# Optimization experiments

Hardware: AMD Instinct MI355X
Metric: run time of the kernel (lower is better)

Reference implementation:

```python
import jax, jax.numpy as jnp
import numpy as np

PAD = 26
H = 1900
B = 256
T_EPI = 25
T_ANT = 64
T_TOT = 153
EMB = 10
IC = 2 * H  # classifier in_channels = 3800


def setup_inputs() -> dict:
    key = jax.random.key(0)
    ks = jax.random.split(key, 16)
    def rn(i, s, sc):
        return jax.random.normal(ks[i], s, jnp.float32) * sc
    inp = {
        "epitope_x": jax.random.randint(ks[0], (B, T_EPI), 0, 26),
        "left_antigen_x": jax.random.randint(ks[1], (B, T_ANT), 0, 26),
        "right_antigen_x": jax.random.randint(ks[2], (B, T_ANT), 0, 26),
        "total_antigen_x": jax.random.randint(ks[3], (B, T_TOT), 0, 26),
        "embed": rn(4, (27, EMB), 0.1),
        "wx": rn(5, (EMB, 4 * H), 0.1),
        "wh": rn(6, (H, 4 * H), 0.02),
        "wmx": rn(7, (EMB, H), 0.1),
        "wmh": rn(8, (H, H), 0.02),
        "b": rn(9, (4 * H,), 0.1),
        "gx": jnp.ones((4 * H,), jnp.float32),
        "gh": jnp.ones((4 * H,), jnp.float32),
        "gmx": jnp.ones((H,), jnp.float32),
        "gmh": jnp.ones((H,), jnp.float32),
        "bn1_gamma": jnp.ones((IC,), jnp.float32),
        "bn1_beta": jnp.zeros((IC,), jnp.float32),
        "bn1_mean": jnp.zeros((IC,), jnp.float32),
        "bn1_var": jnp.ones((IC,), jnp.float32),
        "W1": rn(10, (IC, IC // 10), 0.02),
        "b1": jnp.zeros((IC // 10,), jnp.float32),
        "bn2_gamma": jnp.ones((IC // 10,), jnp.float32),
        "bn2_beta": jnp.zeros((IC // 10,), jnp.float32),
        "bn2_mean": jnp.zeros((IC // 10,), jnp.float32),
        "bn2_var": jnp.ones((IC // 10,), jnp.float32),
        "W2": rn(11, (IC // 10, 1), 0.05),
        "b2": jnp.zeros((1,), jnp.float32),
    }
    return inp


def _wn(w, g):
    # tf.nn.l2_normalize(w, dim=0) * g  (eps 1e-12)
    return w * (g * jax.lax.rsqrt(jnp.maximum(jnp.sum(w * w, axis=0, keepdims=True), 1e-12)))


def _mlstm(xs, wx, wh, wmx, wmh, b):
    # xs: [T, B, E] -> hidden states [B, T, H]
    nB = xs.shape[1]
    def step(carry, x):
        c, h = carry
        m = (x @ wmx) * (h @ wmh)
        z = x @ wx + m @ wh + b
        i, f, o, u = jnp.split(z, 4, axis=1)
        c = jax.nn.sigmoid(f) * c + jax.nn.sigmoid(i) * jnp.tanh(u)
        h = jax.nn.sigmoid(o) * jnp.tanh(c)
        return (c, h), h
    init = (jnp.zeros((nB, H), xs.dtype), jnp.zeros((nB, H), xs.dtype))
    _, hs = jax.lax.scan(step, init, xs)
    return jnp.swapaxes(hs, 0, 1)


def _forward(epitope_x, left_antigen_x, right_antigen_x, total_antigen_x, embed,
             wx, wh, wmx, wmh, b, gx, gh, gmx, gmh,
             bn1_gamma, bn1_beta, bn1_mean, bn1_var, W1, b1,
             bn2_gamma, bn2_beta, bn2_mean, bn2_var, W2, b2):
    wxn = _wn(wx, gx); whn = _wn(wh, gh); wmxn = _wn(wmx, gmx); wmhn = _wn(wmh, gmh)
    epi_len = jnp.sum((epitope_x != PAD).astype(jnp.int32), axis=1)
    left_len = jnp.maximum(jnp.sum((left_antigen_x != PAD).astype(jnp.int32), axis=1), 1)
    right_len = jnp.maximum(jnp.sum((right_antigen_x != PAD).astype(jnp.int32), axis=1), 1)
    tot_len = epi_len + left_len + right_len
    epi_emb = embed[epitope_x]          # [B, 25, 10]
    tot_emb = embed[total_antigen_x]    # [B, 153, 10]
    epi_hs = _mlstm(jnp.swapaxes(epi_emb, 0, 1), wxn, whn, wmxn, wmhn, b)   # [B, 25, H]
    tot_hs = _mlstm(jnp.swapaxes(tot_emb, 0, 1), wxn, whn, wmxn, wmhn, b)   # [B, 153, H]
    ei = jnp.clip(epi_len - 1, 0, epi_hs.shape[1] - 1)
    ti = jnp.clip(tot_len - 1, 0, tot_hs.shape[1] - 1)
    epi_h = jnp.take_along_axis(epi_hs, ei[:, None, None], axis=1)[:, 0]
    tot_h = jnp.take_along_axis(tot_hs, ti[:, None, None], axis=1)[:, 0]
    x = jnp.concatenate([tot_h, epi_h], axis=-1)  # [B, 3800]
    lrelu = lambda v: jnp.where(v >= 0, v, 0.3 * v)
    bn = lambda v, g, bt, m, vv: (v - m) * jax.lax.rsqrt(vv + 1e-3) * g + bt
    x = bn(lrelu(x), bn1_gamma, bn1_beta, bn1_mean, bn1_var)
    x = x @ W1 + b1
    x = bn(lrelu(x), bn2_gamma, bn2_beta, bn2_mean, bn2_var)
    x = x @ W2 + b2
    return x.reshape(-1)


def reference(epitope_x, left_antigen_x, right_antigen_x, total_antigen_x, embed,
              wx, wh, wmx, wmh, b, gx, gh, gmx, gmh,
              bn1_gamma, bn1_beta, bn1_mean, bn1_var, W1, b1,
              bn2_gamma, bn2_beta, bn2_mean, bn2_var, W2, b2):
    return _forward(epitope_x, left_antigen_x, right_antigen_x, total_antigen_x, embed,
                    wx, wh, wmx, wmh, b, gx, gh, gmx, gmh,
                    bn1_gamma, bn1_beta, bn1_mean, bn1_var, W1, b1,
                    bn2_gamma, bn2_beta, bn2_mean, bn2_var, W2, b2)
```

## Files before the change

kernel.cpp:

```cpp
#include <hip/hip_runtime.h>


typedef _Float16 f16;
typedef _Float16 half8 __attribute__((ext_vector_type(8)));
typedef float f32x4 __attribute__((ext_vector_type(4)));

#define H_    1900
#define HP    1920
#define NKA   60
#define NKB   61
#define NKF   120
#define NR    512
#define TT    153
#define TE    25
#define EMB_  10
#define FCN   384

__device__ __forceinline__ float sigm(float x) {
  float p = __expf(-fabsf(x));
  float r = 1.f / (1.f + p);
  return x >= 0.f ? r : 1.f - r;
}
__device__ __forceinline__ float tanh_(float x) {
  float p = __expf(-2.f * fabsf(x));
  float r = (1.f - p) / (1.f + p);
  return x >= 0.f ? r : -r;
}

__device__ __forceinline__ void gll16(const f16* g, f16* l) {
  __builtin_amdgcn_global_load_lds(
      (const __attribute__((address_space(1))) unsigned int*)g,
      (__attribute__((address_space(3))) unsigned int*)l, 16, 0, 0);
}


__global__ void k_norms(const float* __restrict__ wh, const float* __restrict__ wx,
                        const float* __restrict__ wmh, const float* __restrict__ wmx,
                        const float* __restrict__ gh, const float* __restrict__ gx,
                        const float* __restrict__ gmh, const float* __restrict__ gmx,
                        float* __restrict__ inv_wh, float* __restrict__ inv_wx,
                        float* __restrict__ inv_wmh, float* __restrict__ inv_wmx) {
  int tid = blockIdx.x * 256 + threadIdx.x;
  if (tid < 7600) {
    float s = 0.f;
    for (int k = 0; k < H_; k++) { float v = wh[(size_t)k * 7600 + tid]; s += v * v; }
    inv_wh[tid] = gh[tid] * rsqrtf(fmaxf(s, 1e-12f));
  } else if (tid < 15200) {
    int n = tid - 7600; float s = 0.f;
    for (int e = 0; e < EMB_; e++) { float v = wx[(size_t)e * 7600 + n]; s += v * v; }
    inv_wx[n] = gx[n] * rsqrtf(fmaxf(s, 1e-12f));
  } else if (tid < 17100) {
    int n = tid - 15200; float s = 0.f;
    for (int k = 0; k < H_; k++) { float v = wmh[(size_t)k * H_ + n]; s += v * v; }
    inv_wmh[n] = gmh[n] * rsqrtf(fmaxf(s, 1e-12f));
  } else if (tid < 19000) {
    int n = tid - 17100; float s = 0.f;
    for (int e = 0; e < EMB_; e++) { float v = wmx[(size_t)e * H_ + n]; s += v * v; }
    inv_wmx[n] = gmx[n] * rsqrtf(fmaxf(s, 1e-12f));
  }
}

__global__ void k_wmhS(const float* __restrict__ wmh, const float* __restrict__ inv,
                       f16* __restrict__ WmhS) {
  int i = blockIdx.x * 256 + threadIdx.x;
  if (i >= 1920 * 1920) return;
  int n = i % 1920, k = i / 1920;
  float v = (n < H_ && k < H_) ? wmh[(size_t)k * H_ + n] * inv[n] : 0.f;
  int c = n >> 4, nl = n & 15, kb = k >> 5, kl = k & 31;
  WmhS[(((size_t)c * NKA + kb) * 512) + (nl + 16 * (kl >> 3)) * 8 + (kl & 7)] = (f16)v;
}

__global__ void k_whS(const float* __restrict__ wh, const float* __restrict__ wx,
                      const float* __restrict__ bias,
                      const float* __restrict__ inv_wh, const float* __restrict__ inv_wx,
                      f16* __restrict__ WhS) {
  int i = blockIdx.x * 256 + threadIdx.x;
  if (i >= 7600 * 1952) return;
  int col = i % 7600, k = i / 7600;
  float v = 0.f;
  if (k < H_)                        v = wh[(size_t)k * 7600 + col] * inv_wh[col];
  else if (k >= HP && k < HP + EMB_) v = wx[(size_t)(k - HP) * 7600 + col] * inv_wx[col];
  else if (k == HP + EMB_)           v = bias[col];
  int g = col / H_, n = col % H_;
  int q = n >> 4, nl = n & 15, kb = k >> 5, kl = k & 31;
  WhS[(((size_t)(q * 4 + g) * NKB + kb) * 512) + (nl + 16 * (kl >> 3)) * 8 + (kl & 7)] = (f16)v;
}

__global__ void k_wmxT(const float* __restrict__ wmx, const float* __restrict__ inv_wmx,
                       f16* __restrict__ wmxT) {
  int i = blockIdx.x * 256 + threadIdx.x;
  if (i >= HP * 32) return;
  int n = i >> 5, k = i & 31;
  float v = (k < EMB_ && n < H_) ? wmx[(size_t)k * H_ + n] * inv_wmx[n] : 0.f;
  wmxT[i] = (f16)v;
}

__global__ void k_lens(const int* __restrict__ ex, const int* __restrict__ lx,
                       const int* __restrict__ rx, int* __restrict__ sel) {
  int s = threadIdx.x;
  int el = 0; for (int i = 0; i < 25; i++) el += (ex[s * 25 + i] != 26);
  int ll = 0; for (int i = 0; i < 64; i++) ll += (lx[s * 64 + i] != 26);
  int rl = 0; for (int i = 0; i < 64; i++) rl += (rx[s * 64 + i] != 26);
  ll = ll < 1 ? 1 : ll;  rl = rl < 1 ? 1 : rl;
  int tl = el + ll + rl;
  int ti = tl - 1; ti = ti < 0 ? 0 : (ti > 152 ? 152 : ti);
  int ei = el - 1; ei = ei < 0 ? 0 : (ei > 24 ? 24 : ei);
  sel[s] = ti; sel[256 + s] = ei;
}

__global__ void k_init(f16* __restrict__ h0, f16* __restrict__ h1, float* __restrict__ c) {
  int i = blockIdx.x * 256 + threadIdx.x;
  if (i < NR * HP) { h0[i] = (f16)0.f; h1[i] = (f16)0.f; c[i] = 0.f; }
}

__global__ void k_xe16(const int* __restrict__ totx, const int* __restrict__ epix,
                       const float* __restrict__ embed, f16* __restrict__ xe16) {
  int i = blockIdx.x * blockDim.x + threadIdx.x;
  if (i >= TT * NR) return;
  int t = i / NR, r = i % NR;
  int tok = -1;
  if (r < 256) tok = totx[r * TT + t];
  else if (t < TE) tok = epix[(r - 256) * TE + t];
  f16* o = xe16 + (size_t)i * 32;
  #pragma unroll
  for (int e = 0; e < EMB_; e++) o[e] = (f16)(tok >= 0 ? embed[tok * EMB_ + e] : 0.f);
  o[10] = (f16)1.f;
  #pragma unroll
  for (int e = 11; e < 32; e++) o[e] = (f16)0.f;
}


__global__ __launch_bounds__(256, 1)
void k_stepA(const f16* __restrict__ hS, const f16* __restrict__ WmhS,
             const f16* __restrict__ xe16_t, const f16* __restrict__ wmxT,
             f16* __restrict__ mS, int rgc) {
  __shared__ __align__(16) f16 Bb[2][8][4][512];
  const int lane = threadIdx.x & 63, wid = threadIdx.x >> 6;
  const int bi = blockIdx.x;
  const int x = bi & 7, mm = bi >> 3;
  const int rg = mm % rgc, chi = mm / rgc;
  const int ct = chi * 8 + x;
  if (ct >= 30) return;
  const int rtile = rg * 4 + wid;
  const int r0 = rtile * 16;
  const int l16 = lane & 15, l4 = lane >> 4;

  const f16* Abase = hS   + (size_t)rtile * NKA * 512 + lane * 8;
  const f16* Bglob = WmhS + (size_t)(ct * 4) * NKA * 512 + lane * 8;

  f32x4 xm[4];
  {
    half8 xa = *(const half8*)(xe16_t + (size_t)(r0 + l16) * 32 + l4 * 8);
    #pragma unroll
    for (int cb = 0; cb < 4; cb++) {
      half8 xb = *(const half8*)(wmxT + (size_t)(ct * 64 + cb * 16 + l16) * 32 + l4 * 8);
      f32x4 z = {0.f, 0.f, 0.f, 0.f};
      xm[cb] = __builtin_amdgcn_mfma_f32_16x16x32_f16(xa, xb, z, 0, 0, 0);
    }
  }

  half8 Areg[2][8];
  f32x4 acc[4];
  #pragma unroll
  for (int cb = 0; cb < 4; cb++) { f32x4 z = {0.f, 0.f, 0.f, 0.f}; acc[cb] = z; }

#define STAGE_A(g, buf) { const int c0_ = (g) * 8, n_ = ((g) == 7 ? 4 : 8); \
    _Pragma("unroll") for (int q_ = 0; q_ < 8; q_++) { int p_ = wid * 8 + q_; \
      if (p_ < n_ * 4) { int kbl_ = p_ >> 2, cb_ = p_ & 3; \
        gll16(Bglob + ((size_t)cb_ * NKA + c0_ + kbl_) * 512, &Bb[buf][kbl_][cb_][0]); } } }
#define LOADA_A(g, buf) { const int c0_ = (g) * 8, n_ = ((g) == 7 ? 4 : 8); \
    _Pragma("unroll") for (int kk_ = 0; kk_ < 8; kk_++) if (kk_ < n_) \
      Areg[buf][kk_] = *(const half8*)(Abase + (size_t)(c0_ + kk_) * 512); }
#define COMP_A(g, buf) { const int n_ = ((g) == 7 ? 4 : 8); \
    _Pragma("unroll") for (int kk_ = 0; kk_ < 8; kk_++) if (kk_ < n_) { \
      half8 fbv0 = *(const half8*)&Bb[buf][kk_][0][lane * 8]; \
      half8 fbv1 = *(const half8*)&Bb[buf][kk_][1][lane * 8]; \
      half8 fbv2 = *(const half8*)&Bb[buf][kk_][2][lane * 8]; \
      half8 fbv3 = *(const half8*)&Bb[buf][kk_][3][lane * 8]; \
      acc[0] = __builtin_amdgcn_mfma_f32_16x16x32_f16(Areg[buf][kk_], fbv0, acc[0], 0, 0, 0); \
      acc[1] = __builtin_amdgcn_mfma_f32_16x16x32_f16(Areg[buf][kk_], fbv1, acc[1], 0, 0, 0); \
      acc[2] = __builtin_amdgcn_mfma_f32_16x16x32_f16(Areg[buf][kk_], fbv2, acc[2], 0, 0, 0); \
      acc[3] = __builtin_amdgcn_mfma_f32_16x16x32_f16(Areg[buf][kk_], fbv3, acc[3], 0, 0, 0); } }

  LOADA_A(0, 0); STAGE_A(0, 0);
  __syncthreads();
  #pragma unroll
  for (int g = 0; g < 8; g++) {
    if (g < 7) { STAGE_A(g + 1, (g + 1) & 1); LOADA_A(g + 1, (g + 1) & 1); }
    COMP_A(g, g & 1);
    __syncthreads();
  }
#undef STAGE_A
#undef LOADA_A
#undef COMP_A

  const int q4 = lane >> 4, c16 = lane & 15;
  #pragma unroll
  for (int cb = 0; cb < 4; cb++) {
    int kb = ct * 2 + (cb >> 1);
    int klane = (cb & 1) * 16 + c16;
    int lf = (klane >> 3) * 16;
    int sub = c16 & 7;
    f16* dst = mS + ((size_t)rtile * NKB + kb) * 512 + sub;
    #pragma unroll
    for (int q = 0; q < 4; q++) {
      int rl = q4 * 4 + q;
      dst[(rl + lf) * 8] = (f16)(acc[cb][q] * xm[cb][q]);
    }
  }
  if (ct == 0) {
    f16* dst = mS + ((size_t)rtile * NKB + 60) * 512 + lane * 8;
    *(half8*)dst = *(const half8*)(xe16_t + (size_t)(r0 + l16) * 32 + l4 * 8);
  }
}

__global__ __launch_bounds__(256, 1)
void k_stepB(const f16* __restrict__ mS, const f16* __restrict__ WhS,
             float* __restrict__ c, f16* __restrict__ houtS,
             float* __restrict__ selH, const int* __restrict__ sel, int t, int rgc) {
  __shared__ __align__(16) f16 Bb[2][8][4][512];
  const int lane = threadIdx.x & 63, wid = threadIdx.x >> 6;
  const int bi = blockIdx.x;
  const int x = bi & 7, mm = bi >> 3;
  const int rg = mm % rgc, chi = mm / rgc;
  const int colq = chi * 8 + x;
  if (colq >= 119) return;
  const int rt0 = (rg * 4 + wid) * 2;
  const int r0 = rt0 * 16;

  const f16* Abase = mS  + (size_t)rt0 * NKB * 512 + lane * 8;
  const f16* Bglob = WhS + (size_t)(colq * 4) * NKB * 512 + lane * 8;

  half8 Areg[2][8][2];
  f32x4 acc[2][4];
  #pragma unroll
  for (int a = 0; a < 2; a++)
    #pragma unroll
    for (int b = 0; b < 4; b++) { f32x4 z = {0.f, 0.f, 0.f, 0.f}; acc[a][b] = z; }

#define STAGE_B(g, buf) { const int c0_ = (g) * 8, n_ = ((g) == 7 ? 5 : 8); \
    _Pragma("unroll") for (int q_ = 0; q_ < 8; q_++) { int p_ = wid * 8 + q_; \
      if (p_ < n_ * 4) { int kbl_ = p_ >> 2, gg_ = p_ & 3; \
        gll16(Bglob + ((size_t)gg_ * NKB + c0_ + kbl_) * 512, &Bb[buf][kbl_][gg_][0]); } } }
#define LOADA_B(g, buf) { const int c0_ = (g) * 8, n_ = ((g) == 7 ? 5 : 8); \
    _Pragma("unroll") for (int kk_ = 0; kk_ < 8; kk_++) if (kk_ < n_) { \
      Areg[buf][kk_][0] = *(const half8*)(Abase + (size_t)(c0_ + kk_) * 512); \
      Areg[buf][kk_][1] = *(const half8*)(Abase + ((size_t)NKB + c0_ + kk_) * 512); } }
#define COMP_B(g, buf) { const int n_ = ((g) == 7 ? 5 : 8); \
    _Pragma("unroll") for (int kk_ = 0; kk_ < 8; kk_++) if (kk_ < n_) { \
      half8 fbv0 = *(const half8*)&Bb[buf][kk_][0][lane * 8]; \
      half8 fbv1 = *(const half8*)&Bb[buf][kk_][1][lane * 8]; \
      half8 fbv2 = *(const half8*)&Bb[buf][kk_][2][lane * 8]; \
      half8 fbv3 = *(const half8*)&Bb[buf][kk_][3][lane * 8]; \
      _Pragma("unroll") for (int rf_ = 0; rf_ < 2; rf_++) { \
        acc[rf_][0] = __builtin_amdgcn_mfma_f32_16x16x32_f16(Areg[buf][kk_][rf_], fbv0, acc[rf_][0], 0, 0, 0); \
        acc[rf_][1] = __builtin_amdgcn_mfma_f32_16x16x32_f16(Areg[buf][kk_][rf_], fbv1, acc[rf_][1], 0, 0, 0); \
        acc[rf_][2] = __builtin_amdgcn_mfma_f32_16x16x32_f16(Areg[buf][kk_][rf_], fbv2, acc[rf_][2], 0, 0, 0); \
        acc[rf_][3] = __builtin_amdgcn_mfma_f32_16x16x32_f16(Areg[buf][kk_][rf_], fbv3, acc[rf_][3], 0, 0, 0); } } }

  LOADA_B(0, 0); STAGE_B(0, 0);
  __syncthreads();
  #pragma unroll
  for (int g = 0; g < 8; g++) {
    if (g < 7) { STAGE_B(g + 1, (g + 1) & 1); LOADA_B(g + 1, (g + 1) & 1); }
    COMP_B(g, g & 1);
    __syncthreads();
  }
#undef STAGE_B
#undef LOADA_B
#undef COMP_B

  const int q4 = lane >> 4, c16 = lane & 15;
  const int j = colq * 16 + c16;
  const bool valid = j < H_;
  const int kbh = colq >> 1;
  const int lfh = ((((colq & 1) * 16 + c16) >> 3)) * 16;
  const int subh = c16 & 7;
  #pragma unroll
  for (int rf = 0; rf < 2; rf++) {
    f16* hdst = houtS + ((size_t)(rt0 + rf) * NKA + kbh) * 512 + subh;
    #pragma unroll
    for (int q = 0; q < 4; q++) {
      int rl = q4 * 4 + q;
      int row = r0 + rf * 16 + rl;
      if (valid) {
        size_t idx = (size_t)row * HP + j;
        float cold = c[idx];
        float iz = acc[rf][0][q], fz = acc[rf][1][q];
        float oz = acc[rf][2][q], uz = acc[rf][3][q];
        float cn = sigm(fz) * cold + sigm(iz) * tanh_(uz);
        float hv = sigm(oz) * tanh_(cn);
        c[idx] = cn;
        hdst[(rl + lfh) * 8] = (f16)hv;
        if (t == sel[row]) selH[idx] = hv;
      }
    }
  }
}


__global__ void k_xqS(const float* __restrict__ selH, const float* __restrict__ g1,
                      const float* __restrict__ be1, const float* __restrict__ mu1,
                      const float* __restrict__ var1, f16* __restrict__ xqS) {
  int i = blockIdx.x * 256 + threadIdx.x;
  if (i >= 256 * 3840) return;
  int k = i % 3840, s = i / 3840;
  float v = 0.f; bool have = false;
  if (k < H_)            { v = selH[(size_t)s * HP + k]; have = true; }
  else if (k < 2 * H_)   { v = selH[(size_t)(256 + s) * HP + (k - H_)]; have = true; }
  float q = 0.f;
  if (have) {
    float lr = v < 0.f ? 0.3f * v : v;
    q = (lr - mu1[k]) * rsqrtf(var1[k] + 1e-3f) * g1[k] + be1[k];
  }
  int rtile = s >> 4, sl = s & 15, kb = k >> 5, kl = k & 31;
  xqS[(((size_t)rtile * NKF + kb) * 512) + (sl + 16 * (kl >> 3)) * 8 + (kl & 7)] = (f16)q;
}

__global__ void k_w1S(const float* __restrict__ W1, f16* __restrict__ W1S) {
  int i = blockIdx.x * 256 + threadIdx.x;
  if (i >= 384 * 3840) return;
  int col = i % 384, k = i / 384;
  float v = (col < 380 && k < 2 * H_) ? W1[(size_t)k * 380 + col] : 0.f;
  int cg = col >> 4, nl = col & 15, kb = k >> 5, kl = k & 31;
  W1S[(((size_t)cg * NKF + kb) * 512) + (nl + 16 * (kl >> 3)) * 8 + (kl & 7)] = (f16)v;
}

__global__ __launch_bounds__(256)
void k_fc1(const f16* __restrict__ xqS, const f16* __restrict__ W1S,
           const float* __restrict__ b1, float* __restrict__ z1) {
  const int lane = threadIdx.x & 63, wid = threadIdx.x >> 6;
  const int ct = blockIdx.x % 6, rg = blockIdx.x / 6;
  const int rtile = rg * 4 + wid;
  const int r0 = rtile * 16;

  const f16* Abase = xqS + (size_t)rtile * NKF * 512 + lane * 8;
  const f16* Bbase = W1S + (size_t)(ct * 4) * NKF * 512 + lane * 8;

  half8 fa0, fa1, fa2, fa3;
  half8 fb0[4], fb1[4], fb2[4], fb3[4];
  f32x4 acc[4];
  #pragma unroll
  for (int cb = 0; cb < 4; cb++) { f32x4 z = {0.f, 0.f, 0.f, 0.f}; acc[cb] = z; }

#define LDA_F(d, kb)  d = *(const half8*)(Abase + (size_t)(kb) * 512)
#define LDB_F(d, kb)  { _Pragma("unroll") for (int cb = 0; cb < 4; cb++) \
    d[cb] = *(const half8*)(Bbase + ((size_t)cb * NKF + (kb)) * 512); }
#define MMA_F(fa, fb) { _Pragma("unroll") for (int cb = 0; cb < 4; cb++) \
    acc[cb] = __builtin_amdgcn_mfma_f32_16x16x32_f16(fa, fb[cb], acc[cb], 0, 0, 0); }

  LDA_F(fa0, 0); LDB_F(fb0, 0);
  LDA_F(fa1, 1); LDB_F(fb1, 1);
  LDA_F(fa2, 2); LDB_F(fb2, 2);
  for (int base = 0; base < 116; base += 4) {
    LDA_F(fa3, base + 3); LDB_F(fb3, base + 3);
    MMA_F(fa0, fb0);
    LDA_F(fa0, base + 4); LDB_F(fb0, base + 4);
    MMA_F(fa1, fb1);
    LDA_F(fa1, base + 5); LDB_F(fb1, base + 5);
    MMA_F(fa2, fb2);
    LDA_F(fa2, base + 6); LDB_F(fb2, base + 6);
    MMA_F(fa3, fb3);
  }
  LDA_F(fa3, 119); LDB_F(fb3, 119);
  MMA_F(fa0, fb0);
  MMA_F(fa1, fb1);
  MMA_F(fa2, fb2);
  MMA_F(fa3, fb3);
#undef LDA_F
#undef LDB_F
#undef MMA_F

  const int q4 = lane >> 4, c16 = lane & 15;
  #pragma unroll
  for (int cb = 0; cb < 4; cb++)
    #pragma unroll
    for (int q = 0; q < 4; q++) {
      int row = r0 + q4 * 4 + q;
      int col = ct * 64 + cb * 16 + c16;
      float bias = (col < 380) ? b1[col] : 0.f;
      z1[(size_t)row * FCN + col] = acc[cb][q] + bias;
    }
}

__global__ void k_fc2(const float* __restrict__ z1, const float* __restrict__ g2,
                      const float* __restrict__ be2, const float* __restrict__ mu2,
                      const float* __restrict__ var2, const float* __restrict__ W2,
                      const float* __restrict__ b2, float* __restrict__ out) {
  int s = threadIdx.x;
  float a = 0.f;
  for (int jj = 0; jj < 380; jj++) {
    float v = z1[(size_t)s * FCN + jj];
    float lr = v < 0.f ? 0.3f * v : v;
    float q = (lr - mu2[jj]) * rsqrtf(var2[jj] + 1e-3f) * g2[jj] + be2[jj];
    a += q * W2[jj];
  }
  out[s] = a + b2[0];
}


extern "C" void kernel_launch(void* const* d_in, const int* in_sizes, int n_in,
                              void* d_out, int out_size, void* d_ws, size_t ws_size,
                              hipStream_t stream) {
  const int*   epix  = (const int*)d_in[0];
  const int*   lx    = (const int*)d_in[1];
  const int*   rx    = (const int*)d_in[2];
  const int*   totx  = (const int*)d_in[3];
  const float* embed = (const float*)d_in[4];
  const float* wx    = (const float*)d_in[5];
  const float* wh    = (const float*)d_in[6];
  const float* wmx   = (const float*)d_in[7];
  const float* wmh   = (const float*)d_in[8];
  const float* bb    = (const float*)d_in[9];
  const float* gx    = (const float*)d_in[10];
  const float* gh    = (const float*)d_in[11];
  const float* gmx   = (const float*)d_in[12];
  const float* gmh   = (const float*)d_in[13];
  const float* bn1g  = (const float*)d_in[14];
  const float* bn1b  = (const float*)d_in[15];
  const float* bn1m  = (const float*)d_in[16];
  const float* bn1v  = (const float*)d_in[17];
  const float* W1    = (const float*)d_in[18];
  const float* b1    = (const float*)d_in[19];
  const float* bn2g  = (const float*)d_in[20];
  const float* bn2b  = (const float*)d_in[21];
  const float* bn2m  = (const float*)d_in[22];
  const float* bn2v  = (const float*)d_in[23];
  const float* W2    = (const float*)d_in[24];
  const float* b2v   = (const float*)d_in[25];

  char* base = (char*)d_ws;
  size_t off = 0;
  auto alloc = [&](size_t n) { char* p = base + off; off = (off + n + 255) & ~(size_t)255; return p; };

  f16*   WmhS   = (f16*)  alloc((size_t)120 * NKA * 512 * 2);
  f16*   WhS    = (f16*)  alloc((size_t)119 * 4 * NKB * 512 * 2);
  f16*   wmxT   = (f16*)  alloc((size_t)HP * 32 * 2);
  f16*   xe16   = (f16*)  alloc((size_t)TT * NR * 32 * 2);
  f16*   h0S    = (f16*)  alloc((size_t)32 * NKA * 512 * 2);
  f16*   h1S    = (f16*)  alloc((size_t)32 * NKA * 512 * 2);
  f16*   mS     = (f16*)  alloc((size_t)32 * NKB * 512 * 2);
  float* cst    = (float*)alloc((size_t)NR * HP * 4);
  float* selH   = (float*)alloc((size_t)NR * HP * 4);
  int*   sel    = (int*)  alloc((size_t)NR * 4);
  float* inv_wh = (float*)alloc(7600 * 4);
  float* inv_wx = (float*)alloc(7600 * 4);
  float* inv_wmh= (float*)alloc(1900 * 4);
  float* inv_wmx= (float*)alloc(1900 * 4);
  f16*   xqS    = (f16*)  alloc((size_t)16 * NKF * 512 * 2);
  f16*   W1S    = (f16*)  alloc((size_t)24 * NKF * 512 * 2);
  float* z1     = (float*)alloc((size_t)256 * FCN * 4);
  (void)in_sizes; (void)n_in; (void)out_size; (void)ws_size;

  hipLaunchKernelGGL(k_norms, dim3(75), dim3(256), 0, stream,
                     wh, wx, wmh, wmx, gh, gx, gmh, gmx, inv_wh, inv_wx, inv_wmh, inv_wmx);
  hipLaunchKernelGGL(k_wmhS, dim3((1920 * 1920 + 255) / 256), dim3(256), 0, stream,
                     wmh, inv_wmh, WmhS);
  hipLaunchKernelGGL(k_whS, dim3((7600 * 1952 + 255) / 256), dim3(256), 0, stream,
                     wh, wx, bb, inv_wh, inv_wx, WhS);
  hipLaunchKernelGGL(k_wmxT, dim3((HP * 32 + 255) / 256), dim3(256), 0, stream,
                     wmx, inv_wmx, wmxT);
  hipLaunchKernelGGL(k_lens, dim3(1), dim3(256), 0, stream, epix, lx, rx, sel);
  hipLaunchKernelGGL(k_init, dim3((NR * HP + 255) / 256), dim3(256), 0, stream,
                     h0S, h1S, cst);
  hipLaunchKernelGGL(k_xe16, dim3((TT * NR + 255) / 256), dim3(256), 0, stream,
                     totx, epix, embed, xe16);

  for (int t = 0; t < TT; t++) {
    int Mt = (t < TE) ? NR : 256;
    const f16* hin = (t & 1) ? h1S : h0S;
    f16*       ho  = (t & 1) ? h0S : h1S;
    int rgcA = Mt / 64;
    int rgcB = Mt / 128;
    hipLaunchKernelGGL(k_stepA, dim3(8 * rgcA * 4), dim3(256), 0, stream,
                       hin, WmhS, xe16 + (size_t)t * NR * 32, wmxT, mS, rgcA);
    hipLaunchKernelGGL(k_stepB, dim3(8 * rgcB * 15), dim3(256), 0, stream,
                       mS, WhS, cst, ho, selH, sel, t, rgcB);
  }

  hipLaunchKernelGGL(k_xqS, dim3((256 * 3840 + 255) / 256), dim3(256), 0, stream,
                     selH, bn1g, bn1b, bn1m, bn1v, xqS);
  hipLaunchKernelGGL(k_w1S, dim3((384 * 3840 + 255) / 256), dim3(256), 0, stream, W1, W1S);
  hipLaunchKernelGGL(k_fc1, dim3(24), dim3(256), 0, stream, xqS, W1S, b1, z1);
  hipLaunchKernelGGL(k_fc2, dim3(1), dim3(256), 0, stream,
                     z1, bn2g, bn2b, bn2m, bn2v, W2, b2v, (float*)d_out);
}
```

Measured before the change: 5.279 ms.

## Split norm reduction across blocks and halve stepA column tile for more blocks

The weight-norm kernel is split into a partial-sum pass over four K segments (300 blocks) plus a finalize pass, so the long serial column reduction runs on more of the GPU. k_stepA now has each block cover two 16-column subtiles instead of four. This doubles the grid and halves LDS use, and launch bounds are raised to allow two blocks per CU. k_stepB macros are reparameterised with an explicit count but do the same work. The cost is an extra launch, a partial-sum buffer, and A-tile loads repeated across the two column halves.

```diff
diff --git a/kernel.cpp b/kernel.cpp
--- a/kernel.cpp
+++ b/kernel.cpp
@@ -34,30 +34,45 @@
 }
 
 
-__global__ void k_norms(const float* __restrict__ wh, const float* __restrict__ wx,
-                        const float* __restrict__ wmh, const float* __restrict__ wmx,
-                        const float* __restrict__ gh, const float* __restrict__ gx,
-                        const float* __restrict__ gmh, const float* __restrict__ gmx,
-                        float* __restrict__ inv_wh, float* __restrict__ inv_wx,
-                        float* __restrict__ inv_wmh, float* __restrict__ inv_wmx) {
+__global__ void k_norms_p(const float* __restrict__ wh, const float* __restrict__ wx,
+                          const float* __restrict__ wmh, const float* __restrict__ wmx,
+                          float* __restrict__ part) {
+  int seg = blockIdx.x & 3;
+  int tid = (blockIdx.x >> 2) * 256 + threadIdx.x;
+  float s = 0.f;
+  if (tid < 7600) {
+    int k0 = seg * 475;
+    for (int k = k0; k < k0 + 475; k++) { float v = wh[(size_t)k * 7600 + tid]; s += v * v; }
+  } else if (tid < 15200) {
+    if (seg == 0) {
+      int n = tid - 7600;
+      for (int e = 0; e < EMB_; e++) { float v = wx[(size_t)e * 7600 + n]; s += v * v; }
+    }
+  } else if (tid < 17100) {
+    int n = tid - 15200; int k0 = seg * 475;
+    for (int k = k0; k < k0 + 475; k++) { float v = wmh[(size_t)k * H_ + n]; s += v * v; }
+  } else if (tid < 19000) {
+    if (seg == 0) {
+      int n = tid - 17100;
+      for (int e = 0; e < EMB_; e++) { float v = wmx[(size_t)e * H_ + n]; s += v * v; }
+    }
+  }
+  if (tid < 19000) part[(size_t)seg * 19000 + tid] = s;
+}
+
+__global__ void k_norms_f(const float* __restrict__ part,
+                          const float* __restrict__ gh, const float* __restrict__ gx,
+                          const float* __restrict__ gmh, const float* __restrict__ gmx,
+                          float* __restrict__ inv_wh, float* __restrict__ inv_wx,
+                          float* __restrict__ inv_wmh, float* __restrict__ inv_wmx) {
   int tid = blockIdx.x * 256 + threadIdx.x;
-  if (tid < 7600) {
-    float s = 0.f;
-    for (int k = 0; k < H_; k++) { float v = wh[(size_t)k * 7600 + tid]; s += v * v; }
-    inv_wh[tid] = gh[tid] * rsqrtf(fmaxf(s, 1e-12f));
-  } else if (tid < 15200) {
-    int n = tid - 7600; float s = 0.f;
-    for (int e = 0; e < EMB_; e++) { float v = wx[(size_t)e * 7600 + n]; s += v * v; }
-    inv_wx[n] = gx[n] * rsqrtf(fmaxf(s, 1e-12f));
-  } else if (tid < 17100) {
-    int n = tid - 15200; float s = 0.f;
-    for (int k = 0; k < H_; k++) { float v = wmh[(size_t)k * H_ + n]; s += v * v; }
-    inv_wmh[n] = gmh[n] * rsqrtf(fmaxf(s, 1e-12f));
-  } else if (tid < 19000) {
-    int n = tid - 17100; float s = 0.f;
-    for (int e = 0; e < EMB_; e++) { float v = wmx[(size_t)e * H_ + n]; s += v * v; }
-    inv_wmx[n] = gmx[n] * rsqrtf(fmaxf(s, 1e-12f));
-  }
+  if (tid >= 19000) return;
+  float s = part[tid] + part[19000 + tid] + part[38000 + tid] + part[57000 + tid];
+  float r = rsqrtf(fmaxf(s, 1e-12f));
+  if (tid < 7600)        inv_wh[tid] = gh[tid] * r;
+  else if (tid < 15200)  { int n = tid - 7600;  inv_wx[n]  = gx[n]  * r; }
+  else if (tid < 17100)  { int n = tid - 15200; inv_wmh[n] = gmh[n] * r; }
+  else                   { int n = tid - 17100; inv_wmx[n] = gmx[n] * r; }
 }
 
 __global__ void k_wmhS(const float* __restrict__ wmh, const float* __restrict__ inv,
@@ -130,15 +145,16 @@
 }
 
 
-__global__ __launch_bounds__(256, 1)
+__global__ __launch_bounds__(256, 2)
 void k_stepA(const f16* __restrict__ hS, const f16* __restrict__ WmhS,
              const f16* __restrict__ xe16_t, const f16* __restrict__ wmxT,
              f16* __restrict__ mS, int rgc) {
-  __shared__ __align__(16) f16 Bb[2][8][4][512];
+  __shared__ __align__(16) f16 Bb[2][8][2][512];
   const int lane = threadIdx.x & 63, wid = threadIdx.x >> 6;
   const int bi = blockIdx.x;
   const int x = bi & 7, mm = bi >> 3;
-  const int rg = mm % rgc, chi = mm / rgc;
+  const int rg = mm % rgc, rem = mm / rgc;
+  const int cbh = rem & 1, chi = rem >> 1;
   const int ct = chi * 8 + x;
   if (ct >= 30) return;
   const int rtile = rg * 4 + wid;
@@ -146,48 +162,45 @@
   const int l16 = lane & 15, l4 = lane >> 4;
 
   const f16* Abase = hS   + (size_t)rtile * NKA * 512 + lane * 8;
-  const f16* Bglob = WmhS + (size_t)(ct * 4) * NKA * 512 + lane * 8;
-
-  f32x4 xm[4];
+  const f16* Bglob = WmhS + (size_t)(ct * 4 + cbh * 2) * NKA * 512 + lane * 8;
+
+  f32x4 xm[2];
   {
     half8 xa = *(const half8*)(xe16_t + (size_t)(r0 + l16) * 32 + l4 * 8);
     #pragma unroll
-    for (int cb = 0; cb < 4; cb++) {
-      half8 xb = *(const half8*)(wmxT + (size_t)(ct * 64 + cb * 16 + l16) * 32 + l4 * 8);
+    for (int cb = 0; cb < 2; cb++) {
+      half8 xb = *(const half8*)(wmxT + (size_t)(ct * 64 + (cbh * 2 + cb) * 16 + l16) * 32 + l4 * 8);
       f32x4 z = {0.f, 0.f, 0.f, 0.f};
       xm[cb] = __builtin_amdgcn_mfma_f32_16x16x32_f16(xa, xb, z, 0, 0, 0);
     }
   }
 
   half8 Areg[2][8];
-  f32x4 acc[4];
-  #pragma unroll
-  for (int cb = 0; cb < 4; cb++) { f32x4 z = {0.f, 0.f, 0.f, 0.f}; acc[cb] = z; }
-
-#define STAGE_A(g, buf) { const int c0_ = (g) * 8, n_ = ((g) == 7 ? 4 : 8); \
-    _Pragma("unroll") for (int q_ = 0; q_ < 8; q_++) { int p_ = wid * 8 + q_; \
-      if (p_ < n_ * 4) { int kbl_ = p_ >> 2, cb_ = p_ & 3; \
-        gll16(Bglob + ((size_t)cb_ * NKA + c0_ + kbl_) * 512, &Bb[buf][kbl_][cb_][0]); } } }
-#define LOADA_A(g, buf) { const int c0_ = (g) * 8, n_ = ((g) == 7 ? 4 : 8); \
-    _Pragma("unroll") for (int kk_ = 0; kk_ < 8; kk_++) if (kk_ < n_) \
-      Areg[buf][kk_] = *(const half8*)(Abase + (size_t)(c0_ + kk_) * 512); }
-#define COMP_A(g, buf) { const int n_ = ((g) == 7 ? 4 : 8); \
-    _Pragma("unroll") for (int kk_ = 0; kk_ < 8; kk_++) if (kk_ < n_) { \
-      half8 fbv0 = *(const half8*)&Bb[buf][kk_][0][lane * 8]; \
-      half8 fbv1 = *(const half8*)&Bb[buf][kk_][1][lane * 8]; \
-      half8 fbv2 = *(const half8*)&Bb[buf][kk_][2][lane * 8]; \
-      half8 fbv3 = *(const half8*)&Bb[buf][kk_][3][lane * 8]; \
-      acc[0] = __builtin_amdgcn_mfma_f32_16x16x32_f16(Areg[buf][kk_], fbv0, acc[0], 0, 0, 0); \
-      acc[1] = __builtin_amdgcn_mfma_f32_16x16x32_f16(Areg[buf][kk_], fbv1, acc[1], 0, 0, 0); \
-      acc[2] = __builtin_amdgcn_mfma_f32_16x16x32_f16(Areg[buf][kk_], fbv2, acc[2], 0, 0, 0); \
-      acc[3] = __builtin_amdgcn_mfma_f32_16x16x32_f16(Areg[buf][kk_], fbv3, acc[3], 0, 0, 0); } }
-
-  LOADA_A(0, 0); STAGE_A(0, 0);
+  f32x4 acc[2];
+  #pragma unroll
+  for (int cb = 0; cb < 2; cb++) { f32x4 z = {0.f, 0.f, 0.f, 0.f}; acc[cb] = z; }
+
+#define STAGE_A(g, buf, n_) { _Pragma("unroll") for (int q_ = 0; q_ < ((n_) >> 1); q_++) { \
+    int p_ = wid * ((n_) >> 1) + q_; int kbl_ = p_ >> 1, cb_ = p_ & 1; \
+    gll16(Bglob + ((size_t)cb_ * NKA + (g) * 8 + kbl_) * 512, &Bb[buf][kbl_][cb_][0]); } }
+#define LOADA_A(g, buf, n_) { _Pragma("unroll") for (int kk_ = 0; kk_ < 8; kk_++) if (kk_ < (n_)) \
+    Areg[buf][kk_] = *(const half8*)(Abase + (size_t)((g) * 8 + kk_) * 512); }
+#define COMP_A(g, buf, n_) { _Pragma("unroll") for (int kk_ = 0; kk_ < 8; kk_++) if (kk_ < (n_)) { \
+    half8 b0_ = *(const half8*)&Bb[buf][kk_][0][lane * 8]; \
+    half8 b1_ = *(const half8*)&Bb[buf][kk_][1][lane * 8]; \
+    acc[0] = __builtin_amdgcn_mfma_f32_16x16x32_f16(Areg[buf][kk_], b0_, acc[0], 0, 0, 0); \
+    acc[1] = __builtin_amdgcn_mfma_f32_16x16x32_f16(Areg[buf][kk_], b1_, acc[1], 0, 0, 0); } }
+
+  LOADA_A(0, 0, 8); STAGE_A(0, 0, 8);
   __syncthreads();
   #pragma unroll
   for (int g = 0; g < 8; g++) {
-    if (g < 7) { STAGE_A(g + 1, (g + 1) & 1); LOADA_A(g + 1, (g + 1) & 1); }
-    COMP_A(g, g & 1);
+    const int nn = (g == 7) ? 4 : 8;
+    if (g < 7) {
+      const int nn1 = (g == 6) ? 4 : 8;
+      STAGE_A(g + 1, (g + 1) & 1, nn1); LOADA_A(g + 1, (g + 1) & 1, nn1);
+    }
+    COMP_A(g, g & 1, nn);
     __syncthreads();
   }
 #undef STAGE_A
@@ -195,10 +208,10 @@
 #undef COMP_A
 
   const int q4 = lane >> 4, c16 = lane & 15;
-  #pragma unroll
-  for (int cb = 0; cb < 4; cb++) {
-    int kb = ct * 2 + (cb >> 1);
-    int klane = (cb & 1) * 16 + c16;
+  const int kb = ct * 2 + cbh;
+  #pragma unroll
+  for (int cb = 0; cb < 2; cb++) {
+    int klane = cb * 16 + c16;
     int lf = (klane >> 3) * 16;
     int sub = c16 & 7;
     f16* dst = mS + ((size_t)rtile * NKB + kb) * 512 + sub;
@@ -208,7 +221,7 @@
       dst[(rl + lf) * 8] = (f16)(acc[cb][q] * xm[cb][q]);
     }
   }
-  if (ct == 0) {
+  if (ct == 0 && cbh == 0) {
     f16* dst = mS + ((size_t)rtile * NKB + 60) * 512 + lane * 8;
     *(half8*)dst = *(const half8*)(xe16_t + (size_t)(r0 + l16) * 32 + l4 * 8);
   }
@@ -238,32 +251,34 @@
     #pragma unroll
     for (int b = 0; b < 4; b++) { f32x4 z = {0.f, 0.f, 0.f, 0.f}; acc[a][b] = z; }
 
-#define STAGE_B(g, buf) { const int c0_ = (g) * 8, n_ = ((g) == 7 ? 5 : 8); \
-    _Pragma("unroll") for (int q_ = 0; q_ < 8; q_++) { int p_ = wid * 8 + q_; \
-      if (p_ < n_ * 4) { int kbl_ = p_ >> 2, gg_ = p_ & 3; \
-        gll16(Bglob + ((size_t)gg_ * NKB + c0_ + kbl_) * 512, &Bb[buf][kbl_][gg_][0]); } } }
-#define LOADA_B(g, buf) { const int c0_ = (g) * 8, n_ = ((g) == 7 ? 5 : 8); \
-    _Pragma("unroll") for (int kk_ = 0; kk_ < 8; kk_++) if (kk_ < n_) { \
-      Areg[buf][kk_][0] = *(const half8*)(Abase + (size_t)(c0_ + kk_) * 512); \
-      Areg[buf][kk_][1] = *(const half8*)(Abase + ((size_t)NKB + c0_ + kk_) * 512); } }
-#define COMP_B(g, buf) { const int n_ = ((g) == 7 ? 5 : 8); \
-    _Pragma("unroll") for (int kk_ = 0; kk_ < 8; kk_++) if (kk_ < n_) { \
-      half8 fbv0 = *(const half8*)&Bb[buf][kk_][0][lane * 8]; \
-      half8 fbv1 = *(const half8*)&Bb[buf][kk_][1][lane * 8]; \
-      half8 fbv2 = *(const half8*)&Bb[buf][kk_][2][lane * 8]; \
-      half8 fbv3 = *(const half8*)&Bb[buf][kk_][3][lane * 8]; \
-      _Pragma("unroll") for (int rf_ = 0; rf_ < 2; rf_++) { \
-        acc[rf_][0] = __builtin_amdgcn_mfma_f32_16x16x32_f16(Areg[buf][kk_][rf_], fbv0, acc[rf_][0], 0, 0, 0); \
-        acc[rf_][1] = __builtin_amdgcn_mfma_f32_16x16x32_f16(Areg[buf][kk_][rf_], fbv1, acc[rf_][1], 0, 0, 0); \
-        acc[rf_][2] = __builtin_amdgcn_mfma_f32_16x16x32_f16(Areg[buf][kk_][rf_], fbv2, acc[rf_][2], 0, 0, 0); \
-        acc[rf_][3] = __builtin_amdgcn_mfma_f32_16x16x32_f16(Areg[buf][kk_][rf_], fbv3, acc[rf_][3], 0, 0, 0); } } }
-
-  LOADA_B(0, 0); STAGE_B(0, 0);
+#define STAGE_B(g, buf, n_) { _Pragma("unroll") for (int q_ = 0; q_ < 8; q_++) { \
+    int p_ = wid * 8 + q_; \
+    if (p_ < (n_) * 4) { int kbl_ = p_ >> 2, gg_ = p_ & 3; \
+      gll16(Bglob + ((size_t)gg_ * NKB + (g) * 8 + kbl_) * 512, &Bb[buf][kbl_][gg_][0]); } } }
+#define LOADA_B(g, buf, n_) { _Pragma("unroll") for (int kk_ = 0; kk_ < 8; kk_++) if (kk_ < (n_)) { \
+    Areg[buf][kk_][0] = *(const half8*)(Abase + (size_t)((g) * 8 + kk_) * 512); \
+    Areg[buf][kk_][1] = *(const half8*)(Abase + ((size_t)NKB + (g) * 8 + kk_) * 512); } }
+#define COMP_B(g, buf, n_) { _Pragma("unroll") for (int kk_ = 0; kk_ < 8; kk_++) if (kk_ < (n_)) { \
+    half8 b0_ = *(const half8*)&Bb[buf][kk_][0][lane * 8]; \
+    half8 b1_ = *(const half8*)&Bb[buf][kk_][1][lane * 8]; \
+    half8 b2_ = *(const half8*)&Bb[buf][kk_][2][lane * 8]; \
+    half8 b3_ = *(const half8*)&Bb[buf][kk_][3][lane * 8]; \
+    _Pragma("unroll") for (int rf_ = 0; rf_ < 2; rf_++) { \
+      acc[rf_][0] = __builtin_amdgcn_mfma_f32_16x16x32_f16(Areg[buf][kk_][rf_], b0_, acc[rf_][0], 0, 0, 0); \
+      acc[rf_][1] = __builtin_amdgcn_mfma_f32_16x16x32_f16(Areg[buf][kk_][rf_], b1_, acc[rf_][1], 0, 0, 0); \
+      acc[rf_][2] = __builtin_amdgcn_mfma_f32_16x16x32_f16(Areg[buf][kk_][rf_], b2_, acc[rf_][2], 0, 0, 0); \
+      acc[rf_][3] = __builtin_amdgcn_mfma_f32_16x16x32_f16(Areg[buf][kk_][rf_], b3_, acc[rf_][3], 0, 0, 0); } } }
+
+  LOADA_B(0, 0, 8); STAGE_B(0, 0, 8);
   __syncthreads();
   #pragma unroll
   for (int g = 0; g < 8; g++) {
-    if (g < 7) { STAGE_B(g + 1, (g + 1) & 1); LOADA_B(g + 1, (g + 1) & 1); }
-    COMP_B(g, g & 1);
+    const int nn = (g == 7) ? 5 : 8;
+    if (g < 7) {
+      const int nn1 = (g == 6) ? 5 : 8;
+      STAGE_B(g + 1, (g + 1) & 1, nn1); LOADA_B(g + 1, (g + 1) & 1, nn1);
+    }
+    COMP_B(g, g & 1, nn);
     __syncthreads();
   }
 #undef STAGE_B
@@ -447,13 +462,15 @@
   float* inv_wx = (float*)alloc(7600 * 4);
   float* inv_wmh= (float*)alloc(1900 * 4);
   float* inv_wmx= (float*)alloc(1900 * 4);
+  float* npart  = (float*)alloc((size_t)4 * 19000 * 4);
   f16*   xqS    = (f16*)  alloc((size_t)16 * NKF * 512 * 2);
   f16*   W1S    = (f16*)  alloc((size_t)24 * NKF * 512 * 2);
   float* z1     = (float*)alloc((size_t)256 * FCN * 4);
   (void)in_sizes; (void)n_in; (void)out_size; (void)ws_size;
 
-  hipLaunchKernelGGL(k_norms, dim3(75), dim3(256), 0, stream,
-                     wh, wx, wmh, wmx, gh, gx, gmh, gmx, inv_wh, inv_wx, inv_wmh, inv_wmx);
+  hipLaunchKernelGGL(k_norms_p, dim3(300), dim3(256), 0, stream, wh, wx, wmh, wmx, npart);
+  hipLaunchKernelGGL(k_norms_f, dim3(75), dim3(256), 0, stream,
+                     npart, gh, gx, gmh, gmx, inv_wh, inv_wx, inv_wmh, inv_wmx);
   hipLaunchKernelGGL(k_wmhS, dim3((1920 * 1920 + 255) / 256), dim3(256), 0, stream,
                      wmh, inv_wmh, WmhS);
   hipLaunchKernelGGL(k_whS, dim3((7600 * 1952 + 255) / 256), dim3(256), 0, stream,
@@ -472,7 +489,7 @@
     f16*       ho  = (t & 1) ? h0S : h1S;
     int rgcA = Mt / 64;
     int rgcB = Mt / 128;
-    hipLaunchKernelGGL(k_stepA, dim3(8 * rgcA * 4), dim3(256), 0, stream,
+    hipLaunchKernelGGL(k_stepA, dim3(64 * rgcA), dim3(256), 0, stream,
                        hin, WmhS, xe16 + (size_t)t * NR * 32, wmxT, mS, rgcA);
     hipLaunchKernelGGL(k_stepB, dim3(8 * rgcB * 15), dim3(256), 0, stream,
                        mS, WhS, cst, ho, selH, sel, t, rgcB);
```

New measurement: 4.694 ms. 1.12x faster.
